# Kernel tuning notes

Measured on AMD Instinct MI355X. Metric: run time of the kernel, lower is better.

Reference implementation:

```python
import jax, jax.numpy as jnp
import numpy as np

L, D, H, V, T, S_WIN = 6, 512, 2048, 32000, 1024, 64
B = 4
EPS = 1e-5


def layer_norm(x, g, b):
    m = jnp.mean(x, axis=-1, keepdims=True)
    v = jnp.mean(jnp.square(x - m), axis=-1, keepdims=True)
    return (x - m) * jax.lax.rsqrt(v + EPS) * g + b


def aft_local(x, Wq, bq, Wk, bk, Wv, bv, Wo, bo, w_bias, mask):
    # x: [B,T,D]; w_bias: [T,T]; mask: [T,T] bool (causal & local window)
    q = x @ Wq + bq
    k = x @ Wk + bk
    v = x @ Wv + bv
    NEG = jnp.asarray(-1e30, x.dtype)
    wm = jnp.where(mask, w_bias, NEG)                      # [T,T]
    wm = wm - jnp.max(wm, axis=1, keepdims=True)           # row-stable
    ew = jnp.exp(wm)                                       # [T,T], zeros outside window
    ek = jnp.exp(k - jnp.max(k, axis=1, keepdims=True))    # [B,T,D], stable over keys
    num = jnp.einsum('tu,bud->btd', ew, ek * v)
    den = jnp.einsum('tu,bud->btd', ew, ek)
    y = jax.nn.sigmoid(q) * (num / (den + 1e-9))
    return y @ Wo + bo


def setup_inputs() -> dict:
    key = jax.random.key(0)
    ks = jax.random.split(key, 20)
    s = 0.02
    inp = {
        'x': jax.random.randint(ks[0], (B, T), 0, V),
        'tok_emb': jax.random.normal(ks[1], (V, D), jnp.float32) * s,
        'pos_emb': jax.random.normal(ks[2], (T, D), jnp.float32) * s,
        'Wq': jax.random.normal(ks[3], (L, D, D), jnp.float32) * s,
        'bq': jnp.zeros((L, D), jnp.float32),
        'Wk': jax.random.normal(ks[4], (L, D, D), jnp.float32) * s,
        'bk': jnp.zeros((L, D), jnp.float32),
        'Wv': jax.random.normal(ks[5], (L, D, D), jnp.float32) * s,
        'bv': jnp.zeros((L, D), jnp.float32),
        'Wo': jax.random.normal(ks[6], (L, D, D), jnp.float32) * s,
        'bo': jnp.zeros((L, D), jnp.float32),
        'w_bias': jax.random.normal(ks[7], (L, T, T), jnp.float32) * s,
        'ln_g': jnp.ones((L, D), jnp.float32),
        'ln_b': jnp.zeros((L, D), jnp.float32),
        'W1': jax.random.normal(ks[8], (L, D, H), jnp.float32) * s,
        'b1': jnp.zeros((L, H), jnp.float32),
        'W2': jax.random.normal(ks[9], (L, H, D), jnp.float32) * s,
        'b2': jnp.zeros((L, D), jnp.float32),
    }
    return inp


def reference(x, tok_emb, pos_emb, Wq, bq, Wk, bk, Wv, bv, Wo, bo, w_bias,
              ln_g, ln_b, W1, b1, W2, b2):
    scale = jax.lax.rsqrt(jnp.asarray(D, jnp.float32))
    tok = jnp.take(tok_emb, x, axis=0) * scale             # [B,T,D]
    pos = (pos_emb[:x.shape[1]] * scale)[None]             # [1,T,D], broadcast
    h = tok + pos                                          # dropout = identity (eval)

    t = jnp.arange(T)
    mask = (t[:, None] >= t[None, :]) & (t[:, None] - t[None, :] < S_WIN)

    for i in range(L):
        emb = h + pos                                      # source re-adds pos each block
        a = aft_local(emb, Wq[i], bq[i], Wk[i], bk[i], Wv[i], bv[i],
                      Wo[i], bo[i], w_bias[i], mask)
        attn_out = layer_norm(a + emb, ln_g[i], ln_b[i])
        f = jax.nn.relu(attn_out @ W1[i] + b1[i]) @ W2[i] + b2[i]
        h = layer_norm(f + attn_out, ln_g[i], ln_b[i])     # same LN params reused
    return h
```

## Files before the change

kernel.cpp:

```cpp
#include <hip/hip_runtime.h>
#include <hip/hip_bf16.h>

#define BB 4
#define TT 1024
#define DM 512
#define HF 2048
#define NL 6
#define SW 64

constexpr float EMB_SCALE = 0.04419417382415922f;

typedef __attribute__((ext_vector_type(8))) short short8v;
typedef __attribute__((ext_vector_type(4))) float f32x4;

__device__ inline unsigned short f32_to_bf16(float x) {
  union { float f; unsigned u; } c; c.f = x;
  unsigned r = c.u + 0x7fffu + ((c.u >> 16) & 1u);
  return (unsigned short)(r >> 16);
}

__device__ inline void gload16(const void* g, void* l) {
  __builtin_amdgcn_global_load_lds(
      (const __attribute__((address_space(1))) void*)g,
      (__attribute__((address_space(3))) void*)l, 16, 0, 0);
}


__global__ __launch_bounds__(256) void scale_pos_k(const float* __restrict__ pos,
                                                   float* __restrict__ posS) {
  int i = blockIdx.x * 256 + threadIdx.x;
  posS[i] = pos[i] * EMB_SCALE;
}

__global__ __launch_bounds__(256) void embed_k(const int* __restrict__ x,
                                               const float* __restrict__ tok,
                                               const float* __restrict__ posS,
                                               float* __restrict__ h) {
  int i = blockIdx.x * 256 + threadIdx.x;
  int d = i & (DM - 1);
  int bt = i >> 9;
  int t = bt & (TT - 1);
  h[i] = tok[(size_t)x[bt] * DM + d] * EMB_SCALE + posS[t * DM + d];
}

__global__ __launch_bounds__(256) void add_pos_k(const float* __restrict__ h,
                                                 const float* __restrict__ posS,
                                                 float* __restrict__ emb,
                                                 unsigned short* __restrict__ embb) {
  int i = blockIdx.x * 256 + threadIdx.x;
  int d = i & (DM - 1);
  int t = (i >> 9) & (TT - 1);
  float e = h[i] + posS[t * DM + d];
  emb[i] = e;
  embb[i] = f32_to_bf16(e);
}

__global__ __launch_bounds__(256) void transpose_w_k(const float* __restrict__ W,
                                                     unsigned short* __restrict__ Wt,
                                                     int K, int N,
                                                     long out_ls, int out_ro) {
  __shared__ float tile[32][33];
  int l = blockIdx.z;
  const float* Wl = W + (size_t)l * K * N;
  unsigned short* Wtl = Wt + (size_t)l * out_ls;
  int k0 = blockIdx.x * 32, n0 = blockIdx.y * 32;
  int tc = threadIdx.x & 31, tr = threadIdx.x >> 5;
#pragma unroll
  for (int i = 0; i < 4; ++i) {
    int r = tr + i * 8;
    tile[r][tc] = Wl[(size_t)(k0 + r) * N + n0 + tc];
  }
  __syncthreads();
#pragma unroll
  for (int i = 0; i < 4; ++i) {
    int r = tr + i * 8;
    Wtl[(size_t)(out_ro + n0 + r) * K + k0 + tc] = f32_to_bf16(tile[tc][r]);
  }
}

template <int MODE>
__global__ __launch_bounds__(256) void gemm64_k(
    const unsigned short* __restrict__ A,
    const unsigned short* __restrict__ Bt,
    const float* __restrict__ bias,
    float* __restrict__ Cf,
    unsigned short* __restrict__ Cb,
    int M, int N, int K) {
  __shared__ __align__(16) unsigned short Als[64 * 64];
  __shared__ __align__(16) unsigned short Bls[64 * 64];

  const int tid = threadIdx.x;
  const int lane = tid & 63;
  const int wid = tid >> 6;
  const int wm = wid & 1, wn = wid >> 1;
  const int brow = blockIdx.y * 64;
  const int bcol = blockIdx.x * 64;

  f32x4 acc[2][2] = {};

  int p0 = wid * 128 + lane;
  int r0 = p0 >> 3, kb0 = (p0 & 7) ^ (r0 & 7);
  int p1 = p0 + 64;
  int r1 = p1 >> 3, kb1 = (p1 & 7) ^ (r1 & 7);

  const unsigned short* Ag0 = A + (size_t)(brow + r0) * K + kb0 * 8;
  const unsigned short* Ag1 = A + (size_t)(brow + r1) * K + kb1 * 8;
  const unsigned short* Bg0 = Bt + (size_t)(bcol + r0) * K + kb0 * 8;
  const unsigned short* Bg1 = Bt + (size_t)(bcol + r1) * K + kb1 * 8;

  unsigned short* Alp0 = Als + wid * 1024;
  unsigned short* Alp1 = Als + wid * 1024 + 512;
  unsigned short* Blp0 = Bls + wid * 1024;
  unsigned short* Blp1 = Bls + wid * 1024 + 512;

  const int fr = lane & 15;
  const int kg = lane >> 4;

  for (int k0 = 0; k0 < K; k0 += 64) {
    gload16(Ag0 + k0, Alp0);
    gload16(Ag1 + k0, Alp1);
    gload16(Bg0 + k0, Blp0);
    gload16(Bg1 + k0, Blp1);
    __syncthreads();
#pragma unroll
    for (int mk = 0; mk < 2; ++mk) {
      int kb = mk * 4 + kg;
      short8v af[2], bf[2];
#pragma unroll
      for (int i = 0; i < 2; ++i) {
        int ra = wm * 32 + i * 16 + fr;
        int pa = ra * 8 + (kb ^ (ra & 7));
        af[i] = *(const short8v*)(Als + pa * 8);
        int rb = wn * 32 + i * 16 + fr;
        int pb = rb * 8 + (kb ^ (rb & 7));
        bf[i] = *(const short8v*)(Bls + pb * 8);
      }
#pragma unroll
      for (int i = 0; i < 2; ++i)
#pragma unroll
        for (int j = 0; j < 2; ++j)
          acc[i][j] = __builtin_amdgcn_mfma_f32_16x16x32_bf16(af[i], bf[j], acc[i][j], 0, 0, 0);
    }
    __syncthreads();
  }

#pragma unroll
  for (int j = 0; j < 2; ++j) {
    int col = bcol + wn * 32 + j * 16 + fr;
    float bv = bias[col];
#pragma unroll
    for (int i = 0; i < 2; ++i) {
      int rowb = brow + wm * 32 + i * 16 + kg * 4;
#pragma unroll
      for (int r = 0; r < 4; ++r) {
        float v = acc[i][j][r] + bv;
        if (MODE == 1) {
          v = fmaxf(v, 0.f);
          Cb[(size_t)(rowb + r) * N + col] = f32_to_bf16(v);
        } else {
          Cf[(size_t)(rowb + r) * N + col] = v;
        }
      }
    }
  }
}

template <int MODE>
__global__ __launch_bounds__(256) void gemm128_k(
    const unsigned short* __restrict__ A,
    const unsigned short* __restrict__ Bt,
    const float* __restrict__ b0,
    const float* __restrict__ b1,
    const float* __restrict__ b2,
    float* __restrict__ o0,
    float* __restrict__ o1,
    float* __restrict__ o2,
    unsigned short* __restrict__ Cb,
    int M, int N, int K) {
  __shared__ __align__(16) unsigned short Als[128 * 64];
  __shared__ __align__(16) unsigned short Bls[128 * 64];

  const int tid = threadIdx.x;
  const int lane = tid & 63;
  const int wid = tid >> 6;
  const int wm = wid & 1, wn = wid >> 1;
  const int brow = blockIdx.y * 128;
  const int bcol = blockIdx.x * 128;

  f32x4 acc[4][4] = {};

  int rr[4], kk[4];
  const unsigned short* Ag[4];
  const unsigned short* Bg[4];
#pragma unroll
  for (int c = 0; c < 4; ++c) {
    int p = wid * 256 + c * 64 + lane;
    rr[c] = p >> 3;
    kk[c] = (p & 7) ^ (rr[c] & 7);
    Ag[c] = A + (size_t)(brow + rr[c]) * K + kk[c] * 8;
    Bg[c] = Bt + (size_t)(bcol + rr[c]) * K + kk[c] * 8;
  }

  const int fr = lane & 15;
  const int kg = lane >> 4;

  for (int k0 = 0; k0 < K; k0 += 64) {
#pragma unroll
    for (int c = 0; c < 4; ++c) {
      gload16(Ag[c] + k0, Als + wid * 2048 + c * 512);
      gload16(Bg[c] + k0, Bls + wid * 2048 + c * 512);
    }
    __syncthreads();
#pragma unroll
    for (int mk = 0; mk < 2; ++mk) {
      int kb = mk * 4 + kg;
      short8v af[4], bf[4];
#pragma unroll
      for (int i = 0; i < 4; ++i) {
        int ra = wm * 64 + i * 16 + fr;
        int pa = ra * 8 + (kb ^ (ra & 7));
        af[i] = *(const short8v*)(Als + pa * 8);
        int rb = wn * 64 + i * 16 + fr;
        int pb = rb * 8 + (kb ^ (rb & 7));
        bf[i] = *(const short8v*)(Bls + pb * 8);
      }
#pragma unroll
      for (int i = 0; i < 4; ++i)
#pragma unroll
        for (int j = 0; j < 4; ++j)
          acc[i][j] = __builtin_amdgcn_mfma_f32_16x16x32_bf16(af[i], bf[j], acc[i][j], 0, 0, 0);
    }
    __syncthreads();
  }

#pragma unroll
  for (int j = 0; j < 4; ++j) {
    int colg = bcol + wn * 64 + j * 16 + fr;
    float bv;
    float* op;
    int col;
    if (MODE == 2) {
      int sel = colg >> 9;
      col = colg & 511;
      bv = (sel == 0) ? b0[col] : (sel == 1) ? b1[col] : b2[col];
      op = (sel == 0) ? o0 : (sel == 1) ? o1 : o2;
    } else {
      col = colg;
      bv = b0[col];
      op = o0;
    }
    const int ostride = (MODE == 2) ? DM : N;
#pragma unroll
    for (int i = 0; i < 4; ++i) {
      int rowb = brow + wm * 64 + i * 16 + kg * 4;
#pragma unroll
      for (int r = 0; r < 4; ++r) {
        float v = acc[i][j][r] + bv;
        if (MODE == 1) {
          v = fmaxf(v, 0.f);
          Cb[(size_t)(rowb + r) * N + col] = f32_to_bf16(v);
        } else {
          op[(size_t)(rowb + r) * ostride + col] = v;
        }
      }
    }
  }
}


__global__ __launch_bounds__(256) void colmax1_k(const float* __restrict__ k,
                                                 float* __restrict__ pmax) {
  int d = blockIdx.x * 256 + threadIdx.x;
  int b = blockIdx.y;
  int z = blockIdx.z;
  const float* p = k + ((size_t)b * TT + z * 128) * DM + d;
  float m = -1e30f;
#pragma unroll 8
  for (int t = 0; t < 128; ++t) m = fmaxf(m, p[(size_t)t * DM]);
  pmax[((size_t)z * BB + b) * DM + d] = m;
}

__global__ __launch_bounds__(256) void colmax2_k(const float* __restrict__ pmax,
                                                 float* __restrict__ kmax) {
  int d = blockIdx.x * 256 + threadIdx.x;
  int b = blockIdx.y;
  float m = -1e30f;
#pragma unroll
  for (int z = 0; z < 8; ++z) m = fmaxf(m, pmax[((size_t)z * BB + b) * DM + d]);
  kmax[b * DM + d] = m;
}

__global__ __launch_bounds__(256) void exp_kv_k(float* __restrict__ k,
                                                float* __restrict__ v,
                                                const float* __restrict__ kmax) {
  size_t i = (size_t)blockIdx.x * 256 + threadIdx.x;
  int d = (int)(i & (DM - 1));
  int b = (int)(i >> 19);
  float e = __expf(k[i] - kmax[b * DM + d]);
  k[i] = e;
  v[i] = e * v[i];
}

__global__ void ew_prep_k(const float* __restrict__ wb, float* __restrict__ ew) {
  int t = blockIdx.x;
  int j = threadIdx.x;
  int u = t - j;
  bool valid = (u >= 0);
  float w = valid ? wb[(size_t)t * TT + u] : -1e30f;
  float m = w;
#pragma unroll
  for (int off = 32; off; off >>= 1) m = fmaxf(m, __shfl_xor(m, off));
  ew[t * SW + j] = valid ? __expf(w - m) : 0.f;
}

#define AGG_ROWS 127
#define AGG_LDS_BYTES ((AGG_ROWS * 64 * 2 + 64 * 64) * 4)

__global__ __launch_bounds__(256) void aft_agg_k(const float* __restrict__ ek,
                                                 const float* __restrict__ ekv,
                                                 const float* __restrict__ ew,
                                                 const float* __restrict__ q,
                                                 unsigned short* __restrict__ yb) {
  extern __shared__ float smem[];
  float* ekS = smem;
  float* evS = smem + AGG_ROWS * 64;
  float* ewS = smem + AGG_ROWS * 64 * 2;

  const int tid = threadIdx.x;
  const int d0 = blockIdx.x * 64;
  const int t0 = blockIdx.y * 64;
  const int b = blockIdx.z;

  const size_t rowbase = ((size_t)b * TT) * DM + d0;
  for (int idx = tid; idx < AGG_ROWS * 16; idx += 256) {
    int r = idx >> 4, c = idx & 15;
    int u = t0 - 63 + r;
    float4 ze = make_float4(0.f, 0.f, 0.f, 0.f);
    float4 va = (u >= 0) ? *(const float4*)(ek + rowbase + (size_t)u * DM + c * 4) : ze;
    float4 vb = (u >= 0) ? *(const float4*)(ekv + rowbase + (size_t)u * DM + c * 4) : ze;
    *(float4*)(ekS + r * 64 + c * 4) = va;
    *(float4*)(evS + r * 64 + c * 4) = vb;
  }
  for (int idx = tid; idx < 1024; idx += 256) {
    int r = idx >> 4, c = idx & 15;
    *(float4*)(ewS + r * 64 + c * 4) = *(const float4*)(ew + (size_t)(t0 + r) * SW + c * 4);
  }
  __syncthreads();

  const int tx = tid & 63;
  const int ty = tid >> 6;
#pragma unroll
  for (int i = 0; i < 16; ++i) {
    int tl = ty * 16 + i;
    float num = 0.f, den = 0.f;
#pragma unroll 4
    for (int j = 0; j < 64; ++j) {
      float w = ewS[tl * 64 + j];
      int r = tl + 63 - j;
      den += w * ekS[r * 64 + tx];
      num += w * evS[r * 64 + tx];
    }
    size_t base = ((size_t)b * TT + t0 + tl) * DM + d0 + tx;
    float qv = q[base];
    float sig = 1.f / (1.f + __expf(-qv));
    yb[base] = f32_to_bf16(sig * num / (den + 1e-9f));
  }
}

__global__ __launch_bounds__(256) void add_ln_k(const float* __restrict__ X,
                                                const float* __restrict__ Y,
                                                const float* __restrict__ g,
                                                const float* __restrict__ bb,
                                                float* __restrict__ out,
                                                unsigned short* __restrict__ outb) {
  int row = blockIdx.x * 4 + (threadIdx.x >> 6);
  int lane = threadIdx.x & 63;
  const float* x = X + (size_t)row * DM;
  const float* y = Y + (size_t)row * DM;
  float4 v0 = *(const float4*)(x + lane * 8);
  float4 v1 = *(const float4*)(x + lane * 8 + 4);
  float4 w0 = *(const float4*)(y + lane * 8);
  float4 w1 = *(const float4*)(y + lane * 8 + 4);
  float vals[8] = {v0.x + w0.x, v0.y + w0.y, v0.z + w0.z, v0.w + w0.w,
                   v1.x + w1.x, v1.y + w1.y, v1.z + w1.z, v1.w + w1.w};
  float s = 0.f, s2 = 0.f;
#pragma unroll
  for (int i = 0; i < 8; ++i) {
    s += vals[i];
    s2 += vals[i] * vals[i];
  }
#pragma unroll
  for (int off = 32; off; off >>= 1) {
    s += __shfl_xor(s, off);
    s2 += __shfl_xor(s2, off);
  }
  float mean = s * (1.f / DM);
  float var = s2 * (1.f / DM) - mean * mean;
  float rs = rsqrtf(var + 1e-5f);
  float o[8];
#pragma unroll
  for (int i = 0; i < 8; ++i) {
    int d = lane * 8 + i;
    o[i] = (vals[i] - mean) * rs * g[d] + bb[d];
  }
  float* op = out + (size_t)row * DM + lane * 8;
  *(float4*)(op) = make_float4(o[0], o[1], o[2], o[3]);
  *(float4*)(op + 4) = make_float4(o[4], o[5], o[6], o[7]);
  if (outb) {
    unsigned short ob[8];
#pragma unroll
    for (int i = 0; i < 8; ++i) ob[i] = f32_to_bf16(o[i]);
    *(short8v*)(outb + (size_t)row * DM + lane * 8) = *(short8v*)ob;
  }
}


extern "C" void kernel_launch(void* const* d_in, const int* in_sizes, int n_in,
                              void* d_out, int out_size, void* d_ws, size_t ws_size,
                              hipStream_t stream) {
  const int* x = (const int*)d_in[0];
  const float* tok_emb = (const float*)d_in[1];
  const float* pos_emb = (const float*)d_in[2];
  const float* Wq = (const float*)d_in[3];
  const float* bq = (const float*)d_in[4];
  const float* Wk = (const float*)d_in[5];
  const float* bk = (const float*)d_in[6];
  const float* Wv = (const float*)d_in[7];
  const float* bv = (const float*)d_in[8];
  const float* Wo = (const float*)d_in[9];
  const float* bo = (const float*)d_in[10];
  const float* w_bias = (const float*)d_in[11];
  const float* ln_g = (const float*)d_in[12];
  const float* ln_b = (const float*)d_in[13];
  const float* W1 = (const float*)d_in[14];
  const float* b1 = (const float*)d_in[15];
  const float* W2 = (const float*)d_in[16];
  const float* b2 = (const float*)d_in[17];

  const size_t BTD = (size_t)BB * TT * DM;
  char* ws = (char*)d_ws;
  size_t o = 0;
  auto alloc_f = [&](size_t n) { float* p = (float*)(ws + o); o += n * 4; return p; };
  auto alloc_h = [&](size_t n) { unsigned short* p = (unsigned short*)(ws + o); o += n * 2; return p; };

  float* posS = alloc_f((size_t)TT * DM);
  float* h    = alloc_f(BTD);
  float* emb  = alloc_f(BTD);
  float* q    = alloc_f(BTD);
  float* k    = alloc_f(BTD);
  float* v    = alloc_f(BTD);
  float* attn = alloc_f(BTD);
  float* ew   = alloc_f((size_t)TT * SW);
  float* kmax = alloc_f((size_t)BB * DM);
  float* pmax = alloc_f((size_t)8 * BB * DM);
  unsigned short* embb  = alloc_h(BTD);
  unsigned short* yb    = alloc_h(BTD);
  unsigned short* attnb = alloc_h(BTD);
  unsigned short* f1b   = alloc_h((size_t)BB * TT * HF);
  unsigned short* Wqkvt = alloc_h((size_t)NL * 3 * DM * DM);
  unsigned short* Wot = alloc_h((size_t)NL * DM * DM);
  unsigned short* W1t = alloc_h((size_t)NL * DM * HF);
  unsigned short* W2t = alloc_h((size_t)NL * HF * DM);

  const int EW_BLOCKS = (int)(BTD / 256);

  transpose_w_k<<<dim3(DM / 32, DM / 32, NL), 256, 0, stream>>>(Wq, Wqkvt, DM, DM, (long)3 * DM * DM, 0);
  transpose_w_k<<<dim3(DM / 32, DM / 32, NL), 256, 0, stream>>>(Wk, Wqkvt, DM, DM, (long)3 * DM * DM, DM);
  transpose_w_k<<<dim3(DM / 32, DM / 32, NL), 256, 0, stream>>>(Wv, Wqkvt, DM, DM, (long)3 * DM * DM, 2 * DM);
  transpose_w_k<<<dim3(DM / 32, DM / 32, NL), 256, 0, stream>>>(Wo, Wot, DM, DM, (long)DM * DM, 0);
  transpose_w_k<<<dim3(DM / 32, HF / 32, NL), 256, 0, stream>>>(W1, W1t, DM, HF, (long)DM * HF, 0);
  transpose_w_k<<<dim3(HF / 32, DM / 32, NL), 256, 0, stream>>>(W2, W2t, HF, DM, (long)HF * DM, 0);

  scale_pos_k<<<TT * DM / 256, 256, 0, stream>>>(pos_emb, posS);
  embed_k<<<EW_BLOCKS, 256, 0, stream>>>(x, tok_emb, posS, h);

  for (int i = 0; i < NL; ++i) {
    const unsigned short* Wqkvt_i = Wqkvt + (size_t)i * 3 * DM * DM;
    const unsigned short* Wot_i = Wot + (size_t)i * DM * DM;
    const float* bq_i = bq + (size_t)i * DM;
    const float* bk_i = bk + (size_t)i * DM;
    const float* bv_i = bv + (size_t)i * DM;
    const float* bo_i = bo + (size_t)i * DM;
    const float* wb_i = w_bias + (size_t)i * TT * TT;
    const float* g_i = ln_g + (size_t)i * DM;
    const float* b_i = ln_b + (size_t)i * DM;
    const unsigned short* W1t_i = W1t + (size_t)i * DM * HF;
    const float* b1_i = b1 + (size_t)i * HF;
    const unsigned short* W2t_i = W2t + (size_t)i * HF * DM;
    const float* b2_i = b2 + (size_t)i * DM;

    add_pos_k<<<EW_BLOCKS, 256, 0, stream>>>(h, posS, emb, embb);

    gemm128_k<2><<<dim3(3 * DM / 128, BB * TT / 128), 256, 0, stream>>>(
        embb, Wqkvt_i, bq_i, bk_i, bv_i, q, k, v, nullptr, BB * TT, 3 * DM, DM);

    colmax1_k<<<dim3(2, BB, 8), 256, 0, stream>>>(k, pmax);
    colmax2_k<<<dim3(2, BB), 256, 0, stream>>>(pmax, kmax);
    exp_kv_k<<<EW_BLOCKS, 256, 0, stream>>>(k, v, kmax);
    ew_prep_k<<<TT, 64, 0, stream>>>(wb_i, ew);
    aft_agg_k<<<dim3(DM / 64, TT / 64, BB), 256, AGG_LDS_BYTES, stream>>>(k, v, ew, q, yb);

    dim3 g64(DM / 64, BB * TT / 64);
    gemm64_k<0><<<g64, 256, 0, stream>>>(yb, Wot_i, bo_i, k, nullptr, BB * TT, DM, DM);
    add_ln_k<<<BB * TT / 4, 256, 0, stream>>>(k, emb, g_i, b_i, attn, attnb);

    gemm128_k<1><<<dim3(HF / 128, BB * TT / 128), 256, 0, stream>>>(
        attnb, W1t_i, b1_i, nullptr, nullptr, nullptr, nullptr, nullptr, f1b, BB * TT, HF, DM);
    gemm64_k<0><<<g64, 256, 0, stream>>>(f1b, W2t_i, b2_i, v, nullptr, BB * TT, DM, HF);

    float* hout = (i == NL - 1) ? (float*)d_out : h;
    add_ln_k<<<BB * TT / 4, 256, 0, stream>>>(v, attn, g_i, b_i, hout, nullptr);
  }
}
```

Measured before the change: 1.114 ms.

## Fuse pos-add, exp and weight-prep into neighbours; use 128x64 tiles for N=512 GEMMs

```diff
diff --git a/kernel.cpp b/kernel.cpp
--- a/kernel.cpp
+++ b/kernel.cpp
@@ -35,22 +35,13 @@
 __global__ __launch_bounds__(256) void embed_k(const int* __restrict__ x,
                                                const float* __restrict__ tok,
                                                const float* __restrict__ posS,
-                                               float* __restrict__ h) {
+                                               float* __restrict__ emb,
+                                               unsigned short* __restrict__ embb) {
   int i = blockIdx.x * 256 + threadIdx.x;
   int d = i & (DM - 1);
   int bt = i >> 9;
   int t = bt & (TT - 1);
-  h[i] = tok[(size_t)x[bt] * DM + d] * EMB_SCALE + posS[t * DM + d];
-}
-
-__global__ __launch_bounds__(256) void add_pos_k(const float* __restrict__ h,
-                                                 const float* __restrict__ posS,
-                                                 float* __restrict__ emb,
-                                                 unsigned short* __restrict__ embb) {
-  int i = blockIdx.x * 256 + threadIdx.x;
-  int d = i & (DM - 1);
-  int t = (i >> 9) & (TT - 1);
-  float e = h[i] + posS[t * DM + d];
+  float e = tok[(size_t)x[bt] * DM + d] * EMB_SCALE + 2.f * posS[t * DM + d];
   emb[i] = e;
   embb[i] = f32_to_bf16(e);
 }
@@ -75,93 +66,6 @@
   for (int i = 0; i < 4; ++i) {
     int r = tr + i * 8;
     Wtl[(size_t)(out_ro + n0 + r) * K + k0 + tc] = f32_to_bf16(tile[tc][r]);
-  }
-}
-
-template <int MODE>
-__global__ __launch_bounds__(256) void gemm64_k(
-    const unsigned short* __restrict__ A,
-    const unsigned short* __restrict__ Bt,
-    const float* __restrict__ bias,
-    float* __restrict__ Cf,
-    unsigned short* __restrict__ Cb,
-    int M, int N, int K) {
-  __shared__ __align__(16) unsigned short Als[64 * 64];
-  __shared__ __align__(16) unsigned short Bls[64 * 64];
-
-  const int tid = threadIdx.x;
-  const int lane = tid & 63;
-  const int wid = tid >> 6;
-  const int wm = wid & 1, wn = wid >> 1;
-  const int brow = blockIdx.y * 64;
-  const int bcol = blockIdx.x * 64;
-
-  f32x4 acc[2][2] = {};
-
-  int p0 = wid * 128 + lane;
-  int r0 = p0 >> 3, kb0 = (p0 & 7) ^ (r0 & 7);
-  int p1 = p0 + 64;
-  int r1 = p1 >> 3, kb1 = (p1 & 7) ^ (r1 & 7);
-
-  const unsigned short* Ag0 = A + (size_t)(brow + r0) * K + kb0 * 8;
-  const unsigned short* Ag1 = A + (size_t)(brow + r1) * K + kb1 * 8;
-  const unsigned short* Bg0 = Bt + (size_t)(bcol + r0) * K + kb0 * 8;
-  const unsigned short* Bg1 = Bt + (size_t)(bcol + r1) * K + kb1 * 8;
-
-  unsigned short* Alp0 = Als + wid * 1024;
-  unsigned short* Alp1 = Als + wid * 1024 + 512;
-  unsigned short* Blp0 = Bls + wid * 1024;
-  unsigned short* Blp1 = Bls + wid * 1024 + 512;
-
-  const int fr = lane & 15;
-  const int kg = lane >> 4;
-
-  for (int k0 = 0; k0 < K; k0 += 64) {
-    gload16(Ag0 + k0, Alp0);
-    gload16(Ag1 + k0, Alp1);
-    gload16(Bg0 + k0, Blp0);
-    gload16(Bg1 + k0, Blp1);
-    __syncthreads();
-#pragma unroll
-    for (int mk = 0; mk < 2; ++mk) {
-      int kb = mk * 4 + kg;
-      short8v af[2], bf[2];
-#pragma unroll
-      for (int i = 0; i < 2; ++i) {
-        int ra = wm * 32 + i * 16 + fr;
-        int pa = ra * 8 + (kb ^ (ra & 7));
-        af[i] = *(const short8v*)(Als + pa * 8);
-        int rb = wn * 32 + i * 16 + fr;
-        int pb = rb * 8 + (kb ^ (rb & 7));
-        bf[i] = *(const short8v*)(Bls + pb * 8);
-      }
-#pragma unroll
-      for (int i = 0; i < 2; ++i)
-#pragma unroll
-        for (int j = 0; j < 2; ++j)
-          acc[i][j] = __builtin_amdgcn_mfma_f32_16x16x32_bf16(af[i], bf[j], acc[i][j], 0, 0, 0);
-    }
-    __syncthreads();
-  }
-
-#pragma unroll
-  for (int j = 0; j < 2; ++j) {
-    int col = bcol + wn * 32 + j * 16 + fr;
-    float bv = bias[col];
-#pragma unroll
-    for (int i = 0; i < 2; ++i) {
-      int rowb = brow + wm * 32 + i * 16 + kg * 4;
-#pragma unroll
-      for (int r = 0; r < 4; ++r) {
-        float v = acc[i][j][r] + bv;
-        if (MODE == 1) {
-          v = fmaxf(v, 0.f);
-          Cb[(size_t)(rowb + r) * N + col] = f32_to_bf16(v);
-        } else {
-          Cf[(size_t)(rowb + r) * N + col] = v;
-        }
-      }
-    }
   }
 }
 
@@ -267,6 +171,93 @@
   }
 }
 
+__global__ __launch_bounds__(256) void gemmN64_k(
+    const unsigned short* __restrict__ A,
+    const unsigned short* __restrict__ Bt,
+    const float* __restrict__ bias,
+    float* __restrict__ Cf,
+    int M, int N, int K) {
+  __shared__ __align__(16) unsigned short Als[128 * 64];
+  __shared__ __align__(16) unsigned short Bls[64 * 64];
+
+  const int tid = threadIdx.x;
+  const int lane = tid & 63;
+  const int wid = tid >> 6;
+  const int wm = wid & 1, wn = wid >> 1;
+  const int brow = blockIdx.y * 128;
+  const int bcol = blockIdx.x * 64;
+
+  f32x4 acc[4][2] = {};
+
+  int ra_[4], ka_[4], rb_[2], kb_[2];
+  const unsigned short* Ag[4];
+  const unsigned short* Bg[2];
+#pragma unroll
+  for (int c = 0; c < 4; ++c) {
+    int p = wid * 256 + c * 64 + lane;
+    ra_[c] = p >> 3;
+    ka_[c] = (p & 7) ^ (ra_[c] & 7);
+    Ag[c] = A + (size_t)(brow + ra_[c]) * K + ka_[c] * 8;
+  }
+#pragma unroll
+  for (int c = 0; c < 2; ++c) {
+    int p = wid * 128 + c * 64 + lane;
+    rb_[c] = p >> 3;
+    kb_[c] = (p & 7) ^ (rb_[c] & 7);
+    Bg[c] = Bt + (size_t)(bcol + rb_[c]) * K + kb_[c] * 8;
+  }
+
+  const int fr = lane & 15;
+  const int kg = lane >> 4;
+
+  for (int k0 = 0; k0 < K; k0 += 64) {
+#pragma unroll
+    for (int c = 0; c < 4; ++c)
+      gload16(Ag[c] + k0, Als + wid * 2048 + c * 512);
+#pragma unroll
+    for (int c = 0; c < 2; ++c)
+      gload16(Bg[c] + k0, Bls + wid * 1024 + c * 512);
+    __syncthreads();
+#pragma unroll
+    for (int mk = 0; mk < 2; ++mk) {
+      int kb = mk * 4 + kg;
+      short8v af[4], bf[2];
+#pragma unroll
+      for (int i = 0; i < 4; ++i) {
+        int ra = wm * 64 + i * 16 + fr;
+        int pa = ra * 8 + (kb ^ (ra & 7));
+        af[i] = *(const short8v*)(Als + pa * 8);
+      }
+#pragma unroll
+      for (int j = 0; j < 2; ++j) {
+        int rb = wn * 32 + j * 16 + fr;
+        int pb = rb * 8 + (kb ^ (rb & 7));
+        bf[j] = *(const short8v*)(Bls + pb * 8);
+      }
+#pragma unroll
+      for (int i = 0; i < 4; ++i)
+#pragma unroll
+        for (int j = 0; j < 2; ++j)
+          acc[i][j] = __builtin_amdgcn_mfma_f32_16x16x32_bf16(af[i], bf[j], acc[i][j], 0, 0, 0);
+    }
+    __syncthreads();
+  }
+
+#pragma unroll
+  for (int j = 0; j < 2; ++j) {
+    int col = bcol + wn * 32 + j * 16 + fr;
+    float bv = bias[col];
+#pragma unroll
+    for (int i = 0; i < 4; ++i) {
+      int rowb = brow + wm * 64 + i * 16 + kg * 4;
+#pragma unroll
+      for (int r = 0; r < 4; ++r) {
+        Cf[(size_t)(rowb + r) * N + col] = acc[i][j][r] + bv;
+      }
+    }
+  }
+}
+
 
 __global__ __launch_bounds__(256) void colmax1_k(const float* __restrict__ k,
                                                  float* __restrict__ pmax) {
@@ -290,35 +281,13 @@
   kmax[b * DM + d] = m;
 }
 
-__global__ __launch_bounds__(256) void exp_kv_k(float* __restrict__ k,
-                                                float* __restrict__ v,
-                                                const float* __restrict__ kmax) {
-  size_t i = (size_t)blockIdx.x * 256 + threadIdx.x;
-  int d = (int)(i & (DM - 1));
-  int b = (int)(i >> 19);
-  float e = __expf(k[i] - kmax[b * DM + d]);
-  k[i] = e;
-  v[i] = e * v[i];
-}
-
-__global__ void ew_prep_k(const float* __restrict__ wb, float* __restrict__ ew) {
-  int t = blockIdx.x;
-  int j = threadIdx.x;
-  int u = t - j;
-  bool valid = (u >= 0);
-  float w = valid ? wb[(size_t)t * TT + u] : -1e30f;
-  float m = w;
-#pragma unroll
-  for (int off = 32; off; off >>= 1) m = fmaxf(m, __shfl_xor(m, off));
-  ew[t * SW + j] = valid ? __expf(w - m) : 0.f;
-}
-
 #define AGG_ROWS 127
 #define AGG_LDS_BYTES ((AGG_ROWS * 64 * 2 + 64 * 64) * 4)
 
-__global__ __launch_bounds__(256) void aft_agg_k(const float* __restrict__ ek,
-                                                 const float* __restrict__ ekv,
-                                                 const float* __restrict__ ew,
+__global__ __launch_bounds__(256) void aft_agg_k(const float* __restrict__ kr,
+                                                 const float* __restrict__ vr,
+                                                 const float* __restrict__ kmax,
+                                                 const float* __restrict__ wb,
                                                  const float* __restrict__ q,
                                                  unsigned short* __restrict__ yb) {
   extern __shared__ float smem[];
@@ -331,19 +300,45 @@
   const int t0 = blockIdx.y * 64;
   const int b = blockIdx.z;
 
+  {
+    int r = tid >> 2, qq = tid & 3;
+    int t = t0 + r;
+    const float* wrow = wb + (size_t)t * TT + t;
+    float vals[16];
+    float m = -1e30f;
+#pragma unroll
+    for (int jj = 0; jj < 16; ++jj) {
+      int j = qq * 16 + jj;
+      bool valid = (t - j >= 0);
+      vals[jj] = valid ? wrow[-j] : -1e30f;
+      m = fmaxf(m, vals[jj]);
+    }
+    m = fmaxf(m, __shfl_xor(m, 1));
+    m = fmaxf(m, __shfl_xor(m, 2));
+#pragma unroll
+    for (int jj = 0; jj < 16; ++jj) {
+      int j = qq * 16 + jj;
+      ewS[r * 64 + j] = (t - j >= 0) ? __expf(vals[jj] - m) : 0.f;
+    }
+  }
+
   const size_t rowbase = ((size_t)b * TT) * DM + d0;
   for (int idx = tid; idx < AGG_ROWS * 16; idx += 256) {
     int r = idx >> 4, c = idx & 15;
     int u = t0 - 63 + r;
-    float4 ze = make_float4(0.f, 0.f, 0.f, 0.f);
-    float4 va = (u >= 0) ? *(const float4*)(ek + rowbase + (size_t)u * DM + c * 4) : ze;
-    float4 vb = (u >= 0) ? *(const float4*)(ekv + rowbase + (size_t)u * DM + c * 4) : ze;
-    *(float4*)(ekS + r * 64 + c * 4) = va;
-    *(float4*)(evS + r * 64 + c * 4) = vb;
-  }
-  for (int idx = tid; idx < 1024; idx += 256) {
-    int r = idx >> 4, c = idx & 15;
-    *(float4*)(ewS + r * 64 + c * 4) = *(const float4*)(ew + (size_t)(t0 + r) * SW + c * 4);
+    float4 e4 = make_float4(0.f, 0.f, 0.f, 0.f);
+    float4 g4 = make_float4(0.f, 0.f, 0.f, 0.f);
+    if (u >= 0) {
+      float4 k4 = *(const float4*)(kr + rowbase + (size_t)u * DM + c * 4);
+      float4 v4 = *(const float4*)(vr + rowbase + (size_t)u * DM + c * 4);
+      float4 km = *(const float4*)(kmax + (size_t)b * DM + d0 + c * 4);
+      e4.x = __expf(k4.x - km.x); g4.x = e4.x * v4.x;
+      e4.y = __expf(k4.y - km.y); g4.y = e4.y * v4.y;
+      e4.z = __expf(k4.z - km.z); g4.z = e4.z * v4.z;
+      e4.w = __expf(k4.w - km.w); g4.w = e4.w * v4.w;
+    }
+    *(float4*)(ekS + r * 64 + c * 4) = e4;
+    *(float4*)(evS + r * 64 + c * 4) = g4;
   }
   __syncthreads();
 
@@ -367,10 +362,12 @@
   }
 }
 
+template <int ADDPOS>
 __global__ __launch_bounds__(256) void add_ln_k(const float* __restrict__ X,
                                                 const float* __restrict__ Y,
                                                 const float* __restrict__ g,
                                                 const float* __restrict__ bb,
+                                                const float* __restrict__ posS,
                                                 float* __restrict__ out,
                                                 unsigned short* __restrict__ outb) {
   int row = blockIdx.x * 4 + (threadIdx.x >> 6);
@@ -402,6 +399,11 @@
   for (int i = 0; i < 8; ++i) {
     int d = lane * 8 + i;
     o[i] = (vals[i] - mean) * rs * g[d] + bb[d];
+  }
+  if (ADDPOS) {
+    const float* pr = posS + (size_t)(row & (TT - 1)) * DM + lane * 8;
+#pragma unroll
+    for (int i = 0; i < 8; ++i) o[i] += pr[i];
   }
   float* op = out + (size_t)row * DM + lane * 8;
   *(float4*)(op) = make_float4(o[0], o[1], o[2], o[3]);
@@ -444,13 +446,11 @@
   auto alloc_h = [&](size_t n) { unsigned short* p = (unsigned short*)(ws + o); o += n * 2; return p; };
 
   float* posS = alloc_f((size_t)TT * DM);
-  float* h    = alloc_f(BTD);
   float* emb  = alloc_f(BTD);
   float* q    = alloc_f(BTD);
   float* k    = alloc_f(BTD);
   float* v    = alloc_f(BTD);
   float* attn = alloc_f(BTD);
-  float* ew   = alloc_f((size_t)TT * SW);
   float* kmax = alloc_f((size_t)BB * DM);
   float* pmax = alloc_f((size_t)8 * BB * DM);
   unsigned short* embb  = alloc_h(BTD);
@@ -472,7 +472,7 @@
   transpose_w_k<<<dim3(HF / 32, DM / 32, NL), 256, 0, stream>>>(W2, W2t, HF, DM, (long)HF * DM, 0);
 
   scale_pos_k<<<TT * DM / 256, 256, 0, stream>>>(pos_emb, posS);
-  embed_k<<<EW_BLOCKS, 256, 0, stream>>>(x, tok_emb, posS, h);
+  embed_k<<<EW_BLOCKS, 256, 0, stream>>>(x, tok_emb, posS, emb, embb);
 
   for (int i = 0; i < NL; ++i) {
     const unsigned short* Wqkvt_i = Wqkvt + (size_t)i * 3 * DM * DM;
@@ -489,26 +489,28 @@
     const unsigned short* W2t_i = W2t + (size_t)i * HF * DM;
     const float* b2_i = b2 + (size_t)i * DM;
 
-    add_pos_k<<<EW_BLOCKS, 256, 0, stream>>>(h, posS, emb, embb);
-
     gemm128_k<2><<<dim3(3 * DM / 128, BB * TT / 128), 256, 0, stream>>>(
         embb, Wqkvt_i, bq_i, bk_i, bv_i, q, k, v, nullptr, BB * TT, 3 * DM, DM);
 
     colmax1_k<<<dim3(2, BB, 8), 256, 0, stream>>>(k, pmax);
     colmax2_k<<<dim3(2, BB), 256, 0, stream>>>(pmax, kmax);
-    exp_kv_k<<<EW_BLOCKS, 256, 0, stream>>>(k, v, kmax);
-    ew_prep_k<<<TT, 64, 0, stream>>>(wb_i, ew);
-    aft_agg_k<<<dim3(DM / 64, TT / 64, BB), 256, AGG_LDS_BYTES, stream>>>(k, v, ew, q, yb);
-
-    dim3 g64(DM / 64, BB * TT / 64);
-    gemm64_k<0><<<g64, 256, 0, stream>>>(yb, Wot_i, bo_i, k, nullptr, BB * TT, DM, DM);
-    add_ln_k<<<BB * TT / 4, 256, 0, stream>>>(k, emb, g_i, b_i, attn, attnb);
+
+    aft_agg_k<<<dim3(DM / 64, TT / 64, BB), 256, AGG_LDS_BYTES, stream>>>(
+        k, v, kmax, wb_i, q, yb);
+
+    gemmN64_k<<<dim3(DM / 64, BB * TT / 128), 256, 0, stream>>>(
+        yb, Wot_i, bo_i, q, BB * TT, DM, DM);
+    add_ln_k<0><<<BB * TT / 4, 256, 0, stream>>>(q, emb, g_i, b_i, nullptr, attn, attnb);
 
     gemm128_k<1><<<dim3(HF / 128, BB * TT / 128), 256, 0, stream>>>(
         attnb, W1t_i, b1_i, nullptr, nullptr, nullptr, nullptr, nullptr, f1b, BB * TT, HF, DM);
-    gemm64_k<0><<<g64, 256, 0, stream>>>(f1b, W2t_i, b2_i, v, nullptr, BB * TT, DM, HF);
-
-    float* hout = (i == NL - 1) ? (float*)d_out : h;
-    add_ln_k<<<BB * TT / 4, 256, 0, stream>>>(v, attn, g_i, b_i, hout, nullptr);
-  }
-}
+    gemmN64_k<<<dim3(DM / 64, BB * TT / 128), 256, 0, stream>>>(
+        f1b, W2t_i, b2_i, k, BB * TT, DM, HF);
+
+    if (i == NL - 1) {
+      add_ln_k<0><<<BB * TT / 4, 256, 0, stream>>>(k, attn, g_i, b_i, nullptr, (float*)d_out, nullptr);
+    } else {
+      add_ln_k<1><<<BB * TT / 4, 256, 0, stream>>>(k, attn, g_i, b_i, posS, emb, embb);
+    }
+  }
+}
```

Result: no change. 1.105 ms (-0.8%).
